# Kernel tuning notes

Hardware: AMD Instinct MI355X
Metric: run time of the kernel (lower is better)

The kernel has to match this reference:

```python
import jax, jax.numpy as jnp
import numpy as np

EPS = 1e-5
H = W = 14  # spatial grid, N = H*W = 196


def layernorm(x, g, b):
    m = x.mean(-1, keepdims=True)
    v = ((x - m) ** 2).mean(-1, keepdims=True)
    return (x - m) * jax.lax.rsqrt(v + EPS) * g + b


def fem_step(x, s):
    # x: [B, C, H, W]; blockwise instance-norm -> sigmoid gate -> 0.5*x + 0.5*attn*x
    B, C, h, w = x.shape
    nbh = -(-h // s)
    nbw = -(-w // s)
    idh = np.arange(h) // s
    idw = np.arange(w) // s
    bid_np = (idh[:, None] * nbw + idw[None, :]).reshape(-1)  # [h*w]
    cnt = jnp.asarray(np.bincount(bid_np, minlength=nbh * nbw).astype(np.float32))
    bid = jnp.asarray(bid_np)
    xt = x.reshape(B, C, h * w).transpose(2, 0, 1)  # [HW, B, C]
    s1 = jax.ops.segment_sum(xt, bid, num_segments=nbh * nbw)      # [nblk, B, C]
    s2 = jax.ops.segment_sum(xt * xt, bid, num_segments=nbh * nbw)
    mean = s1 / cnt[:, None, None]
    var = s2 / cnt[:, None, None] - mean * mean  # biased var, as F.instance_norm
    attn = jax.nn.sigmoid((xt - mean[bid]) * jax.lax.rsqrt(var[bid] + EPS))
    out = 0.5 * xt * (1.0 + attn)  # 0.5*x + 0.5*attn*x
    return out.transpose(1, 2, 0).reshape(B, C, h, w)


def fem(x):
    # p=[2,1,0] -> block sizes H//4=3, H//2=7, H//1=14
    for s in (H // 4, H // 2, H):
        x = fem_step(x, s)
    return x


def setup_inputs() -> dict:
    key = jax.random.key(0)
    ks = jax.random.split(key, 4)
    B, N, C = 64, H * W, 1024
    hid = 4 * C
    return {
        "x": jax.random.normal(ks[0], (B, N, C), jnp.float32),
        "ln1_g": jnp.ones((C,), jnp.float32),
        "ln1_b": jnp.zeros((C,), jnp.float32),
        "cw": jax.random.normal(ks[1], (H, W // 2 + 1, C, 2), jnp.float32) * 0.02,
        "ln2_g": jnp.ones((C,), jnp.float32),
        "ln2_b": jnp.zeros((C,), jnp.float32),
        "fc1_w": jax.random.normal(ks[2], (C, hid), jnp.float32) * 0.02,
        "fc1_b": jnp.zeros((hid,), jnp.float32),
        "fc2_w": jax.random.normal(ks[3], (hid, C), jnp.float32) * 0.02,
        "fc2_b": jnp.zeros((C,), jnp.float32),
    }


def reference(x, ln1_g, ln1_b, cw, ln2_g, ln2_b, fc1_w, fc1_b, fc2_w, fc2_b):
    B, N, C = x.shape
    # FFT global filter
    y = layernorm(x, ln1_g, ln1_b)
    yf = jnp.fft.rfft2(y.reshape(B, H, W, C), axes=(1, 2), norm="ortho")
    yf = yf * (cw[..., 0] + 1j * cw[..., 1])
    y = jnp.fft.irfft2(yf, s=(H, W), axes=(1, 2), norm="ortho").reshape(B, N, C)
    # MLP
    y = layernorm(y, ln2_g, ln2_b)
    y = jax.nn.gelu(y @ fc1_w + fc1_b, approximate=False) @ fc2_w + fc2_b
    # FEM on [B, C, H, W]
    y = fem(y.transpose(0, 2, 1).reshape(B, C, H, W))
    y = y.reshape(B, C, N).transpose(0, 2, 1)
    return x + y
```

## Files before the change

### kernel.cpp

```cpp
#include <hip/hip_runtime.h>

constexpr int CB = 64;
constexpr int CHH = 14, CWW = 14;
constexpr int CN = 196;
constexpr int CC = 1024;
constexpr int CROWS = CB * CN;
constexpr int CKW = 8;

constexpr float C14[14] = {
  1.0f, 0.9009688679024191f, 0.6234898018587336f, 0.2225209339563144f,
  -0.2225209339563144f, -0.6234898018587336f, -0.9009688679024191f, -1.0f,
  -0.9009688679024191f, -0.6234898018587336f, -0.2225209339563144f,
  0.2225209339563144f, 0.6234898018587336f, 0.9009688679024191f };
constexpr float S14[14] = {
  0.0f, 0.4338837391175581f, 0.7818314824680298f, 0.9749279121818236f,
  0.9749279121818236f, 0.7818314824680298f, 0.4338837391175581f, 0.0f,
  -0.4338837391175581f, -0.7818314824680298f, -0.9749279121818236f,
  -0.9749279121818236f, -0.7818314824680298f, -0.4338837391175581f };

typedef __attribute__((ext_vector_type(8))) short bf16x8;
typedef __attribute__((ext_vector_type(4))) float f32x4;

__device__ __forceinline__ unsigned short f2bf(float f) {
  unsigned u = __builtin_bit_cast(unsigned, f);
  u += 0x7FFFu + ((u >> 16) & 1u);
  return (unsigned short)(u >> 16);
}
__device__ __forceinline__ float bf2f(unsigned short h) {
  return __builtin_bit_cast(float, (unsigned)h << 16);
}

__device__ __forceinline__ void gload_lds16(const void* g, void* l) {
  __builtin_amdgcn_global_load_lds(
      (const __attribute__((address_space(1))) void*)g,
      (__attribute__((address_space(3))) void*)l, 16, 0, 0);
}

#define WAITV(N)  asm volatile("s_waitcnt vmcnt(" #N ")" ::: "memory")

template<int OUTBF>
__global__ __launch_bounds__(256)
void ln_kernel(const float* __restrict__ in, const float* __restrict__ gam,
               const float* __restrict__ bet, float* __restrict__ outf,
               unsigned short* __restrict__ outb)
{
  const int row = blockIdx.x;
  const int t = threadIdx.x;
  const float4 v = *(const float4*)(in + (size_t)row * CC + t * 4);
  float s  = v.x + v.y + v.z + v.w;
  float s2 = v.x*v.x + v.y*v.y + v.z*v.z + v.w*v.w;
  #pragma unroll
  for (int o = 32; o > 0; o >>= 1) { s += __shfl_down(s, o); s2 += __shfl_down(s2, o); }
  __shared__ float red[8];
  const int wid = t >> 6, lane = t & 63;
  if (lane == 0) { red[wid] = s; red[4 + wid] = s2; }
  __syncthreads();
  s  = red[0] + red[1] + red[2] + red[3];
  s2 = red[4] + red[5] + red[6] + red[7];
  const float mean = s * (1.0f / CC);
  const float var  = s2 * (1.0f / CC) - mean * mean;
  const float r = rsqrtf(var + 1e-5f);
  const float4 g4 = *(const float4*)(gam + t * 4);
  const float4 b4 = *(const float4*)(bet + t * 4);
  const float o0 = (v.x - mean) * r * g4.x + b4.x;
  const float o1 = (v.y - mean) * r * g4.y + b4.y;
  const float o2 = (v.z - mean) * r * g4.z + b4.z;
  const float o3 = (v.w - mean) * r * g4.w + b4.w;
  if (OUTBF) {
    ushort4 p; p.x = f2bf(o0); p.y = f2bf(o1); p.z = f2bf(o2); p.w = f2bf(o3);
    *(ushort4*)(outb + (size_t)row * CC + t * 4) = p;
  } else {
    *(float4*)(outf + (size_t)row * CC + t * 4) = make_float4(o0, o1, o2, o3);
  }
}

__global__ __launch_bounds__(256)
void fft_w_fwd(const float* __restrict__ y, float* __restrict__ Ar, float* __restrict__ Ai)
{
  const int t = threadIdx.x;
  const int bid = blockIdx.x;
  const int cc = bid & 3;
  const int tmp = bid >> 2;
  const int h = tmp % 14;
  const int b = tmp / 14;
  const int c = cc * 256 + t;
  const size_t base = ((size_t)b * CN + (size_t)h * CWW) * CC + c;
  float v[14];
  #pragma unroll
  for (int w = 0; w < 14; w++) v[w] = y[base + (size_t)w * CC];
  const size_t obase = (((size_t)b * CHH + h) * CKW) * CC + c;
  #pragma unroll
  for (int kw = 0; kw < 8; kw++) {
    float sr = 0.f, si = 0.f;
    #pragma unroll
    for (int w = 0; w < 14; w++) {
      const int m = (w * kw) % 14;
      sr += v[w] * C14[m];
      si -= v[w] * S14[m];
    }
    Ar[obase + (size_t)kw * CC] = sr;
    Ai[obase + (size_t)kw * CC] = si;
  }
}

__global__ __launch_bounds__(256)
void fft_h_filt(const float* __restrict__ Ar, const float* __restrict__ Ai,
                const float* __restrict__ cw, float* __restrict__ Br, float* __restrict__ Bi)
{
  const int t = threadIdx.x;
  const int bid = blockIdx.x;
  const int cc = bid & 3;
  const int tmp = bid >> 2;
  const int kw = tmp & 7;
  const int b = tmp >> 3;
  const int c = cc * 256 + t;
  const size_t base = (((size_t)b * CHH) * CKW + kw) * CC + c;
  float ar[14], ai[14];
  #pragma unroll
  for (int h = 0; h < 14; h++) {
    ar[h] = Ar[base + (size_t)h * (CKW * CC)];
    ai[h] = Ai[base + (size_t)h * (CKW * CC)];
  }
  float fr[14], fi[14];
  #pragma unroll
  for (int kh = 0; kh < 14; kh++) {
    float yr = 0.f, yi = 0.f;
    #pragma unroll
    for (int h = 0; h < 14; h++) {
      const int m = (h * kh) % 14;
      yr += ar[h] * C14[m] + ai[h] * S14[m];
      yi += ai[h] * C14[m] - ar[h] * S14[m];
    }
    const size_t widx = (((size_t)kh * CKW + kw) * CC + c) * 2;
    const float wr = cw[widx], wi = cw[widx + 1];
    fr[kh] = yr * wr - yi * wi;
    fi[kh] = yr * wi + yi * wr;
  }
  #pragma unroll
  for (int h = 0; h < 14; h++) {
    float sr = 0.f, si = 0.f;
    #pragma unroll
    for (int kh = 0; kh < 14; kh++) {
      const int m = (h * kh) % 14;
      sr += fr[kh] * C14[m] - fi[kh] * S14[m];
      si += fr[kh] * S14[m] + fi[kh] * C14[m];
    }
    Br[base + (size_t)h * (CKW * CC)] = sr;
    Bi[base + (size_t)h * (CKW * CC)] = si;
  }
}

__global__ __launch_bounds__(256)
void fft_w_inv(const float* __restrict__ Br, const float* __restrict__ Bi, float* __restrict__ y2)
{
  const int t = threadIdx.x;
  const int bid = blockIdx.x;
  const int cc = bid & 3;
  const int tmp = bid >> 2;
  const int h = tmp % 14;
  const int b = tmp / 14;
  const int c = cc * 256 + t;
  const size_t ibase = (((size_t)b * CHH + h) * CKW) * CC + c;
  float br[8], bi[8];
  #pragma unroll
  for (int k = 0; k < 8; k++) {
    br[k] = Br[ibase + (size_t)k * CC];
    bi[k] = Bi[ibase + (size_t)k * CC];
  }
  const size_t obase = ((size_t)b * CN + (size_t)h * CWW) * CC + c;
  #pragma unroll
  for (int w = 0; w < 14; w++) {
    float s = br[0] + ((w & 1) ? -br[7] : br[7]);
    #pragma unroll
    for (int k = 1; k < 7; k++) {
      const int m = (w * k) % 14;
      s += 2.0f * (br[k] * C14[m] - bi[k] * S14[m]);
    }
    y2[obase + (size_t)w * CC] = s * (1.0f / 196.0f);
  }
}

__global__ __launch_bounds__(256)
void transpose_f32_bf16(const float* __restrict__ in, unsigned short* __restrict__ out,
                        int R, int Ccols)
{
  __shared__ float tile[32][33];
  const int tx = threadIdx.x & 31;
  const int ty = threadIdx.x >> 5;
  const int cb = blockIdx.x * 32;
  const int rb = blockIdx.y * 32;
  #pragma unroll
  for (int i = 0; i < 32; i += 8)
    tile[ty + i][tx] = in[(size_t)(rb + ty + i) * Ccols + cb + tx];
  __syncthreads();
  #pragma unroll
  for (int i = 0; i < 32; i += 8)
    out[(size_t)(cb + ty + i) * R + rb + tx] = f2bf(tile[tx][ty + i]);
}

template<int DO_GELU>
__global__ __launch_bounds__(256, 4)
void gemm128(const unsigned short* __restrict__ A, const unsigned short* __restrict__ BT,
             const float* __restrict__ bias, unsigned short* __restrict__ C,
             int M, int N, int K)
{
  __shared__ __align__(16) char sA[8192];
  __shared__ __align__(16) char sB[8192];
  const int t = threadIdx.x;
  const int wid = t >> 6, lane = t & 63;
  const int wm = wid >> 1, wn = wid & 1;
  const int lrow = lane & 15, qk = lane >> 4;
  const int dq = qk << 4;

  const int nbx = N >> 7, nby = M >> 7;
  const int per = nbx << 3;
  const int fullg = nby >> 3;
  int by, bx;
  if ((int)blockIdx.x < fullg * per) {
    const int g = blockIdx.x / per, r = blockIdx.x % per;
    by = (g << 3) + (r & 7); bx = r >> 3;
  } else {
    const int r = blockIdx.x - fullg * per;
    const int rem = nby - (fullg << 3);
    by = (fullg << 3) + r % rem; bx = r / rem;
  }
  const int brow = by << 7, bcol = bx << 7;

  const int lr1  = t >> 3;
  const int pp   = (t & 7) << 4;
  const int s1   = pp ^ ((lr1 & 7) << 4);
  const int row1 = (lr1 << 1) + (s1 >> 6);
  const int col1 = (s1 & 63) >> 1;
  const size_t aoff1 = (size_t)(brow + row1) * K + col1;
  const size_t aoff2 = (size_t)(brow + row1 + 64) * K + col1;
  const size_t boff1 = (size_t)(bcol + row1) * K + col1;
  const size_t boff2 = (size_t)(bcol + row1 + 64) * K + col1;
  char* dstA1 = sA + t * 16; char* dstA2 = sA + 4096 + t * 16;
  char* dstB1 = sB + t * 16; char* dstB2 = sB + 4096 + t * 16;

  f32x4 acc[4][4] = {};

  for (int k0 = 0; k0 < K; k0 += 32) {
    __syncthreads();
    gload_lds16(A  + aoff1 + k0, dstA1);
    gload_lds16(A  + aoff2 + k0, dstA2);
    gload_lds16(BT + boff1 + k0, dstB1);
    gload_lds16(BT + boff2 + k0, dstB2);
    WAITV(0);
    __syncthreads();
    bf16x8 af[4], bf[4];
    #pragma unroll
    for (int mf = 0; mf < 4; ++mf) {
      const int row = wm * 64 + mf * 16 + lrow;
      af[mf] = *(const bf16x8*)(sA + (row >> 1) * 128 +
                ((((row & 1) << 6) | dq) ^ (((row >> 1) & 7) << 4)));
    }
    #pragma unroll
    for (int nf = 0; nf < 4; ++nf) {
      const int row = wn * 64 + nf * 16 + lrow;
      bf[nf] = *(const bf16x8*)(sB + (row >> 1) * 128 +
                ((((row & 1) << 6) | dq) ^ (((row >> 1) & 7) << 4)));
    }
    #pragma unroll
    for (int mf = 0; mf < 4; ++mf)
      #pragma unroll
      for (int nf = 0; nf < 4; ++nf)
        acc[mf][nf] = __builtin_amdgcn_mfma_f32_16x16x32_bf16(af[mf], bf[nf],
                                                              acc[mf][nf], 0, 0, 0);
  }

  #pragma unroll
  for (int mf = 0; mf < 4; ++mf) {
    #pragma unroll
    for (int nf = 0; nf < 4; ++nf) {
      const int ccol = bcol + wn * 64 + nf * 16 + lrow;
      const float bb = bias[ccol];
      #pragma unroll
      for (int j = 0; j < 4; ++j) {
        const int r = brow + wm * 64 + mf * 16 + qk * 4 + j;
        float v = acc[mf][nf][j] + bb;
        if (DO_GELU) v = 0.5f * v * (1.0f + erff(v * 0.70710678118654752f));
        C[(size_t)r * N + ccol] = f2bf(v);
      }
    }
  }
}

__device__ __forceinline__ void fem_block(unsigned short* col, int t,
                                          int h0, int nh, int w0, int nw)
{
  float s = 0.f, s2 = 0.f;
  for (int ih = 0; ih < nh; ih++)
    for (int iw = 0; iw < nw; iw++) {
      const float v = bf2f(col[((h0 + ih) * 14 + w0 + iw) * 128 + t]);
      s += v; s2 += v * v;
    }
  const float inv = 1.0f / (float)(nh * nw);
  const float m = s * inv;
  const float var = s2 * inv - m * m;
  const float r = rsqrtf(var + 1e-5f);
  for (int ih = 0; ih < nh; ih++)
    for (int iw = 0; iw < nw; iw++) {
      const int idx = ((h0 + ih) * 14 + w0 + iw) * 128 + t;
      const float v = bf2f(col[idx]);
      const float a = 1.0f / (1.0f + __expf(-(v - m) * r));
      col[idx] = f2bf(0.5f * v * (1.0f + a));
    }
}

__global__ __launch_bounds__(128)
void fem_kernel(const unsigned short* __restrict__ z, const float* __restrict__ x,
                float* __restrict__ out)
{
  __shared__ unsigned short buf[CN * 128];
  const int t = threadIdx.x;
  const int b = blockIdx.x >> 3;
  const int cc = blockIdx.x & 7;
  const int c = cc * 128 + t;
  const size_t base = (size_t)b * CN * CC + c;
  #pragma unroll 4
  for (int n = 0; n < CN; n++) buf[n * 128 + t] = z[base + (size_t)n * CC];
  const int st3[5] = {0, 3, 6, 9, 12};
  const int ln3[5] = {3, 3, 3, 3, 2};
  for (int i = 0; i < 5; i++)
    for (int j = 0; j < 5; j++)
      fem_block(buf, t, st3[i], ln3[i], st3[j], ln3[j]);
  for (int i = 0; i < 2; i++)
    for (int j = 0; j < 2; j++)
      fem_block(buf, t, i * 7, 7, j * 7, 7);
  fem_block(buf, t, 0, 14, 0, 14);
  #pragma unroll 4
  for (int n = 0; n < CN; n++)
    out[base + (size_t)n * CC] = x[base + (size_t)n * CC] + bf2f(buf[n * 128 + t]);
}

extern "C" void kernel_launch(void* const* d_in, const int* in_sizes, int n_in,
                              void* d_out, int out_size, void* d_ws, size_t ws_size,
                              hipStream_t stream) {
  const float* x     = (const float*)d_in[0];
  const float* ln1_g = (const float*)d_in[1];
  const float* ln1_b = (const float*)d_in[2];
  const float* cw    = (const float*)d_in[3];
  const float* ln2_g = (const float*)d_in[4];
  const float* ln2_b = (const float*)d_in[5];
  const float* fc1_w = (const float*)d_in[6];
  const float* fc1_b = (const float*)d_in[7];
  const float* fc2_w = (const float*)d_in[8];
  const float* fc2_b = (const float*)d_in[9];
  float* out = (float*)d_out;
  char* ws = (char*)d_ws;

  const size_t SZ_A = (size_t)CB * CHH * CKW * CC * 4;
  float* Ar = (float*)(ws);
  float* Ai = (float*)(ws + SZ_A);
  float* Br = (float*)(ws + 2 * SZ_A);
  float* Bi = (float*)(ws + 3 * SZ_A);
  unsigned short* A1   = (unsigned short*)(ws);
  unsigned short* W1T  = (unsigned short*)(ws + SZ_A);
  unsigned short* W2T  = (unsigned short*)(ws + SZ_A + (size_t)4096 * 1024 * 2);
  unsigned short* Hmid = (unsigned short*)(ws + 2 * SZ_A);
  unsigned short* Z    = (unsigned short*)(ws);

  ln_kernel<0><<<CROWS, 256, 0, stream>>>(x, ln1_g, ln1_b, out, nullptr);
  fft_w_fwd<<<CB * CHH * 4, 256, 0, stream>>>(out, Ar, Ai);
  fft_h_filt<<<CB * CKW * 4, 256, 0, stream>>>(Ar, Ai, cw, Br, Bi);
  fft_w_inv<<<CB * CHH * 4, 256, 0, stream>>>(Br, Bi, out);
  ln_kernel<1><<<CROWS, 256, 0, stream>>>(out, ln2_g, ln2_b, nullptr, A1);
  transpose_f32_bf16<<<dim3(4096 / 32, 1024 / 32), 256, 0, stream>>>(fc1_w, W1T, 1024, 4096);
  transpose_f32_bf16<<<dim3(1024 / 32, 4096 / 32), 256, 0, stream>>>(fc2_w, W2T, 4096, 1024);
  gemm128<1><<<dim3(3136), 256, 0, stream>>>(A1, W1T, fc1_b, Hmid, CROWS, 4096, 1024);
  gemm128<0><<<dim3(784), 256, 0, stream>>>(Hmid, W2T, fc2_b, Z, CROWS, 1024, 4096);
  fem_kernel<<<CB * 8, 128, 0, stream>>>(Z, x, out);
}
```

Measured before the change: 504.7 us.

## Store FFT intermediates in bf16 and use 128x64 tiles for fc2 GEMM

The layernorm, FFT stages and inverse FFT now read and write bf16 intermediates instead of fp32, which halves the memory traffic of the spectral filter pipeline. The workspace layout is rearranged to match. A new 128x64-tile GEMM kernel doubles the block count for the fc2 projection (784 to 1568 blocks) so more CUs stay busy. The cost is extra rounding error in the FFT path.

```diff
diff --git a/kernel.cpp b/kernel.cpp
--- a/kernel.cpp
+++ b/kernel.cpp
@@ -38,15 +38,20 @@
 
 #define WAITV(N)  asm volatile("s_waitcnt vmcnt(" #N ")" ::: "memory")
 
-template<int OUTBF>
+template<int INBF>
 __global__ __launch_bounds__(256)
-void ln_kernel(const float* __restrict__ in, const float* __restrict__ gam,
-               const float* __restrict__ bet, float* __restrict__ outf,
-               unsigned short* __restrict__ outb)
+void ln_kernel(const void* __restrict__ in_, const float* __restrict__ gam,
+               const float* __restrict__ bet, unsigned short* __restrict__ outb)
 {
   const int row = blockIdx.x;
   const int t = threadIdx.x;
-  const float4 v = *(const float4*)(in + (size_t)row * CC + t * 4);
+  float4 v;
+  if (INBF) {
+    const ushort4 u = ((const ushort4*)in_)[(size_t)row * 256 + t];
+    v = make_float4(bf2f(u.x), bf2f(u.y), bf2f(u.z), bf2f(u.w));
+  } else {
+    v = ((const float4*)in_)[(size_t)row * 256 + t];
+  }
   float s  = v.x + v.y + v.z + v.w;
   float s2 = v.x*v.x + v.y*v.y + v.z*v.z + v.w*v.w;
   #pragma unroll
@@ -62,20 +67,17 @@
   const float r = rsqrtf(var + 1e-5f);
   const float4 g4 = *(const float4*)(gam + t * 4);
   const float4 b4 = *(const float4*)(bet + t * 4);
-  const float o0 = (v.x - mean) * r * g4.x + b4.x;
-  const float o1 = (v.y - mean) * r * g4.y + b4.y;
-  const float o2 = (v.z - mean) * r * g4.z + b4.z;
-  const float o3 = (v.w - mean) * r * g4.w + b4.w;
-  if (OUTBF) {
-    ushort4 p; p.x = f2bf(o0); p.y = f2bf(o1); p.z = f2bf(o2); p.w = f2bf(o3);
-    *(ushort4*)(outb + (size_t)row * CC + t * 4) = p;
-  } else {
-    *(float4*)(outf + (size_t)row * CC + t * 4) = make_float4(o0, o1, o2, o3);
-  }
+  ushort4 p;
+  p.x = f2bf((v.x - mean) * r * g4.x + b4.x);
+  p.y = f2bf((v.y - mean) * r * g4.y + b4.y);
+  p.z = f2bf((v.z - mean) * r * g4.z + b4.z);
+  p.w = f2bf((v.w - mean) * r * g4.w + b4.w);
+  *(ushort4*)(outb + (size_t)row * CC + t * 4) = p;
 }
 
 __global__ __launch_bounds__(256)
-void fft_w_fwd(const float* __restrict__ y, float* __restrict__ Ar, float* __restrict__ Ai)
+void fft_w_fwd(const unsigned short* __restrict__ y,
+               unsigned short* __restrict__ Ar, unsigned short* __restrict__ Ai)
 {
   const int t = threadIdx.x;
   const int bid = blockIdx.x;
@@ -87,7 +89,7 @@
   const size_t base = ((size_t)b * CN + (size_t)h * CWW) * CC + c;
   float v[14];
   #pragma unroll
-  for (int w = 0; w < 14; w++) v[w] = y[base + (size_t)w * CC];
+  for (int w = 0; w < 14; w++) v[w] = bf2f(y[base + (size_t)w * CC]);
   const size_t obase = (((size_t)b * CHH + h) * CKW) * CC + c;
   #pragma unroll
   for (int kw = 0; kw < 8; kw++) {
@@ -98,14 +100,15 @@
       sr += v[w] * C14[m];
       si -= v[w] * S14[m];
     }
-    Ar[obase + (size_t)kw * CC] = sr;
-    Ai[obase + (size_t)kw * CC] = si;
+    Ar[obase + (size_t)kw * CC] = f2bf(sr);
+    Ai[obase + (size_t)kw * CC] = f2bf(si);
   }
 }
 
 __global__ __launch_bounds__(256)
-void fft_h_filt(const float* __restrict__ Ar, const float* __restrict__ Ai,
-                const float* __restrict__ cw, float* __restrict__ Br, float* __restrict__ Bi)
+void fft_h_filt(const unsigned short* __restrict__ Ar, const unsigned short* __restrict__ Ai,
+                const float* __restrict__ cw,
+                unsigned short* __restrict__ Br, unsigned short* __restrict__ Bi)
 {
   const int t = threadIdx.x;
   const int bid = blockIdx.x;
@@ -118,8 +121,8 @@
   float ar[14], ai[14];
   #pragma unroll
   for (int h = 0; h < 14; h++) {
-    ar[h] = Ar[base + (size_t)h * (CKW * CC)];
-    ai[h] = Ai[base + (size_t)h * (CKW * CC)];
+    ar[h] = bf2f(Ar[base + (size_t)h * (CKW * CC)]);
+    ai[h] = bf2f(Ai[base + (size_t)h * (CKW * CC)]);
   }
   float fr[14], fi[14];
   #pragma unroll
@@ -145,13 +148,14 @@
       sr += fr[kh] * C14[m] - fi[kh] * S14[m];
       si += fr[kh] * S14[m] + fi[kh] * C14[m];
     }
-    Br[base + (size_t)h * (CKW * CC)] = sr;
-    Bi[base + (size_t)h * (CKW * CC)] = si;
+    Br[base + (size_t)h * (CKW * CC)] = f2bf(sr);
+    Bi[base + (size_t)h * (CKW * CC)] = f2bf(si);
   }
 }
 
 __global__ __launch_bounds__(256)
-void fft_w_inv(const float* __restrict__ Br, const float* __restrict__ Bi, float* __restrict__ y2)
+void fft_w_inv(const unsigned short* __restrict__ Br, const unsigned short* __restrict__ Bi,
+               unsigned short* __restrict__ y2)
 {
   const int t = threadIdx.x;
   const int bid = blockIdx.x;
@@ -164,8 +168,8 @@
   float br[8], bi[8];
   #pragma unroll
   for (int k = 0; k < 8; k++) {
-    br[k] = Br[ibase + (size_t)k * CC];
-    bi[k] = Bi[ibase + (size_t)k * CC];
+    br[k] = bf2f(Br[ibase + (size_t)k * CC]);
+    bi[k] = bf2f(Bi[ibase + (size_t)k * CC]);
   }
   const size_t obase = ((size_t)b * CN + (size_t)h * CWW) * CC + c;
   #pragma unroll
@@ -176,7 +180,7 @@
       const int m = (w * k) % 14;
       s += 2.0f * (br[k] * C14[m] - bi[k] * S14[m]);
     }
-    y2[obase + (size_t)w * CC] = s * (1.0f / 196.0f);
+    y2[obase + (size_t)w * CC] = f2bf(s * (1.0f / 196.0f));
   }
 }
 
@@ -281,6 +285,89 @@
         float v = acc[mf][nf][j] + bb;
         if (DO_GELU) v = 0.5f * v * (1.0f + erff(v * 0.70710678118654752f));
         C[(size_t)r * N + ccol] = f2bf(v);
+      }
+    }
+  }
+}
+
+__global__ __launch_bounds__(256, 6)
+void gemm128x64(const unsigned short* __restrict__ A, const unsigned short* __restrict__ BT,
+                const float* __restrict__ bias, unsigned short* __restrict__ C,
+                int M, int N, int K)
+{
+  __shared__ __align__(16) char sA[8192];
+  __shared__ __align__(16) char sB[4096];
+  const int t = threadIdx.x;
+  const int wid = t >> 6, lane = t & 63;
+  const int wm = wid >> 1, wn = wid & 1;
+  const int lrow = lane & 15, qk = lane >> 4;
+  const int dq = qk << 4;
+
+  const int nbx = N >> 6, nby = M >> 7;
+  const int per = nbx << 2;
+  const int fullg = nby >> 2;
+  int by, bx;
+  if ((int)blockIdx.x < fullg * per) {
+    const int g = blockIdx.x / per, r = blockIdx.x % per;
+    by = (g << 2) + (r & 3); bx = r >> 2;
+  } else {
+    const int r = blockIdx.x - fullg * per;
+    const int rem = nby - (fullg << 2);
+    by = (fullg << 2) + r % rem; bx = r / rem;
+  }
+  const int brow = by << 7, bcol = bx << 6;
+
+  const int lr1  = t >> 3;
+  const int pp   = (t & 7) << 4;
+  const int s1   = pp ^ ((lr1 & 7) << 4);
+  const int row1 = (lr1 << 1) + (s1 >> 6);
+  const int col1 = (s1 & 63) >> 1;
+  const size_t aoff1 = (size_t)(brow + row1) * K + col1;
+  const size_t aoff2 = (size_t)(brow + row1 + 64) * K + col1;
+  const size_t boff1 = (size_t)(bcol + row1) * K + col1;
+  char* dstA1 = sA + t * 16; char* dstA2 = sA + 4096 + t * 16;
+  char* dstB1 = sB + t * 16;
+
+  f32x4 acc[4][2] = {};
+
+  for (int k0 = 0; k0 < K; k0 += 32) {
+    __syncthreads();
+    gload_lds16(A  + aoff1 + k0, dstA1);
+    gload_lds16(A  + aoff2 + k0, dstA2);
+    gload_lds16(BT + boff1 + k0, dstB1);
+    WAITV(0);
+    __syncthreads();
+    bf16x8 af[4], bf[2];
+    #pragma unroll
+    for (int mf = 0; mf < 4; ++mf) {
+      const int row = wm * 64 + mf * 16 + lrow;
+      af[mf] = *(const bf16x8*)(sA + (row >> 1) * 128 +
+                ((((row & 1) << 6) | dq) ^ (((row >> 1) & 7) << 4)));
+    }
+    #pragma unroll
+    for (int nf = 0; nf < 2; ++nf) {
+      const int row = wn * 32 + nf * 16 + lrow;
+      bf[nf] = *(const bf16x8*)(sB + (row >> 1) * 128 +
+                ((((row & 1) << 6) | dq) ^ (((row >> 1) & 7) << 4)));
+    }
+    #pragma unroll
+    for (int mf = 0; mf < 4; ++mf)
+      #pragma unroll
+      for (int nf = 0; nf < 2; ++nf)
+        acc[mf][nf] = __builtin_amdgcn_mfma_f32_16x16x32_bf16(af[mf], bf[nf],
+                                                              acc[mf][nf], 0, 0, 0);
+  }
+
+  #pragma unroll
+  for (int mf = 0; mf < 4; ++mf) {
+    #pragma unroll
+    for (int nf = 0; nf < 2; ++nf) {
+      const int ccol = bcol + wn * 32 + nf * 16 + lrow;
+      const float bb = bias[ccol];
+      #pragma unroll
+      for (int j = 0; j < 4; ++j) {
+        const int r = brow + wm * 64 + mf * 16 + qk * 4 + j;
+        C[(size_t)r * N + ccol] = f2bf(acc[mf][nf][j] + bb);
       }
     }
   }
@@ -350,25 +437,26 @@
   float* out = (float*)d_out;
   char* ws = (char*)d_ws;
 
-  const size_t SZ_A = (size_t)CB * CHH * CKW * CC * 4;
-  float* Ar = (float*)(ws);
-  float* Ai = (float*)(ws + SZ_A);
-  float* Br = (float*)(ws + 2 * SZ_A);
-  float* Bi = (float*)(ws + 3 * SZ_A);
+  const size_t S = (size_t)CB * CHH * CKW * CC * 2;
+  unsigned short* Ar = (unsigned short*)(ws);
+  unsigned short* Ai = (unsigned short*)(ws + S);
+  unsigned short* Br = (unsigned short*)(ws + 2 * S);
+  unsigned short* Bi = (unsigned short*)(ws + 3 * S);
   unsigned short* A1   = (unsigned short*)(ws);
-  unsigned short* W1T  = (unsigned short*)(ws + SZ_A);
-  unsigned short* W2T  = (unsigned short*)(ws + SZ_A + (size_t)4096 * 1024 * 2);
-  unsigned short* Hmid = (unsigned short*)(ws + 2 * SZ_A);
+  unsigned short* W1T  = (unsigned short*)(ws + 2 * S);
+  unsigned short* W2T  = (unsigned short*)(ws + 2 * S + (size_t)4096 * 1024 * 2);
+  unsigned short* Hmid = (unsigned short*)(ws + 2 * S + (size_t)4096 * 1024 * 4);
   unsigned short* Z    = (unsigned short*)(ws);
-
-  ln_kernel<0><<<CROWS, 256, 0, stream>>>(x, ln1_g, ln1_b, out, nullptr);
-  fft_w_fwd<<<CB * CHH * 4, 256, 0, stream>>>(out, Ar, Ai);
+  unsigned short* y12  = (unsigned short*)d_out;
+
+  ln_kernel<0><<<CROWS, 256, 0, stream>>>(x, ln1_g, ln1_b, y12);
+  fft_w_fwd<<<CB * CHH * 4, 256, 0, stream>>>(y12, Ar, Ai);
   fft_h_filt<<<CB * CKW * 4, 256, 0, stream>>>(Ar, Ai, cw, Br, Bi);
-  fft_w_inv<<<CB * CHH * 4, 256, 0, stream>>>(Br, Bi, out);
-  ln_kernel<1><<<CROWS, 256, 0, stream>>>(out, ln2_g, ln2_b, nullptr, A1);
+  fft_w_inv<<<CB * CHH * 4, 256, 0, stream>>>(Br, Bi, y12);
+  ln_kernel<1><<<CROWS, 256, 0, stream>>>(y12, ln2_g, ln2_b, A1);
   transpose_f32_bf16<<<dim3(4096 / 32, 1024 / 32), 256, 0, stream>>>(fc1_w, W1T, 1024, 4096);
   transpose_f32_bf16<<<dim3(1024 / 32, 4096 / 32), 256, 0, stream>>>(fc2_w, W2T, 4096, 1024);
   gemm128<1><<<dim3(3136), 256, 0, stream>>>(A1, W1T, fc1_b, Hmid, CROWS, 4096, 1024);
-  gemm128<0><<<dim3(784), 256, 0, stream>>>(Hmid, W2T, fc2_b, Z, CROWS, 1024, 4096);
+  gemm128x64<<<dim3(1568), 256, 0, stream>>>(Hmid, W2T, fc2_b, Z, CROWS, 1024, 4096);
   fem_kernel<<<CB * 8, 128, 0, stream>>>(Z, x, out);
 }
```

Result: slower. 524.5 us (+3.9%).

## Store FFT intermediates in packed bf16 and deepen GEMM K-tile to 64

Applied to the files above, without the earlier changes.

The layernorm and FFT stages now keep their intermediates in bf16, with real and imaginary parts packed into one 32-bit word. Each thread handles 4 or 2 channels with vector loads, and fewer blocks are launched. The aim is to roughly halve the memory traffic of the memory-bound FFT and layernorm pipeline. Separately, the GEMM stages 64-wide K tiles in double-size LDS with a new swizzle, which halves the loop iterations and barriers. In exchange, FFT precision drops to bf16, and the larger LDS footprint may reduce GEMM occupancy.

```diff
diff --git a/kernel.cpp b/kernel.cpp
--- a/kernel.cpp
+++ b/kernel.cpp
@@ -29,6 +29,9 @@
 __device__ __forceinline__ float bf2f(unsigned short h) {
   return __builtin_bit_cast(float, (unsigned)h << 16);
 }
+__device__ __forceinline__ unsigned pack2(float re, float im) {
+  return (unsigned)f2bf(re) | ((unsigned)f2bf(im) << 16);
+}
 
 __device__ __forceinline__ void gload_lds16(const void* g, void* l) {
   __builtin_amdgcn_global_load_lds(
@@ -38,15 +41,20 @@
 
 #define WAITV(N)  asm volatile("s_waitcnt vmcnt(" #N ")" ::: "memory")
 
-template<int OUTBF>
-__global__ __launch_bounds__(256)
-void ln_kernel(const float* __restrict__ in, const float* __restrict__ gam,
-               const float* __restrict__ bet, float* __restrict__ outf,
-               unsigned short* __restrict__ outb)
+template<int INBF>
+__global__ __launch_bounds__(256)
+void ln_kernel(const void* __restrict__ in_, const float* __restrict__ gam,
+               const float* __restrict__ bet, unsigned short* __restrict__ outb)
 {
   const int row = blockIdx.x;
   const int t = threadIdx.x;
-  const float4 v = *(const float4*)(in + (size_t)row * CC + t * 4);
+  float4 v;
+  if (INBF) {
+    const ushort4 u = ((const ushort4*)in_)[(size_t)row * 256 + t];
+    v = make_float4(bf2f(u.x), bf2f(u.y), bf2f(u.z), bf2f(u.w));
+  } else {
+    v = ((const float4*)in_)[(size_t)row * 256 + t];
+  }
   float s  = v.x + v.y + v.z + v.w;
   float s2 = v.x*v.x + v.y*v.y + v.z*v.z + v.w*v.w;
   #pragma unroll
@@ -62,121 +70,139 @@
   const float r = rsqrtf(var + 1e-5f);
   const float4 g4 = *(const float4*)(gam + t * 4);
   const float4 b4 = *(const float4*)(bet + t * 4);
-  const float o0 = (v.x - mean) * r * g4.x + b4.x;
-  const float o1 = (v.y - mean) * r * g4.y + b4.y;
-  const float o2 = (v.z - mean) * r * g4.z + b4.z;
-  const float o3 = (v.w - mean) * r * g4.w + b4.w;
-  if (OUTBF) {
-    ushort4 p; p.x = f2bf(o0); p.y = f2bf(o1); p.z = f2bf(o2); p.w = f2bf(o3);
-    *(ushort4*)(outb + (size_t)row * CC + t * 4) = p;
-  } else {
-    *(float4*)(outf + (size_t)row * CC + t * 4) = make_float4(o0, o1, o2, o3);
-  }
-}
-
-__global__ __launch_bounds__(256)
-void fft_w_fwd(const float* __restrict__ y, float* __restrict__ Ar, float* __restrict__ Ai)
+  ushort4 p;
+  p.x = f2bf((v.x - mean) * r * g4.x + b4.x);
+  p.y = f2bf((v.y - mean) * r * g4.y + b4.y);
+  p.z = f2bf((v.z - mean) * r * g4.z + b4.z);
+  p.w = f2bf((v.w - mean) * r * g4.w + b4.w);
+  *(ushort4*)(outb + (size_t)row * CC + t * 4) = p;
+}
+
+__global__ __launch_bounds__(256)
+void fft_w_fwd(const unsigned short* __restrict__ y, unsigned* __restrict__ Az)
 {
   const int t = threadIdx.x;
   const int bid = blockIdx.x;
-  const int cc = bid & 3;
-  const int tmp = bid >> 2;
-  const int h = tmp % 14;
-  const int b = tmp / 14;
-  const int c = cc * 256 + t;
-  const size_t base = ((size_t)b * CN + (size_t)h * CWW) * CC + c;
-  float v[14];
-  #pragma unroll
-  for (int w = 0; w < 14; w++) v[w] = y[base + (size_t)w * CC];
-  const size_t obase = (((size_t)b * CHH + h) * CKW) * CC + c;
+  const int h = bid % 14;
+  const int b = bid / 14;
+  const int c4 = t * 4;
+  const size_t base = ((size_t)b * CN + (size_t)h * CWW) * CC + c4;
+  float v[14][4];
+  #pragma unroll
+  for (int w = 0; w < 14; w++) {
+    const ushort4 u = *(const ushort4*)(y + base + (size_t)w * CC);
+    v[w][0] = bf2f(u.x); v[w][1] = bf2f(u.y); v[w][2] = bf2f(u.z); v[w][3] = bf2f(u.w);
+  }
+  const size_t obase = (((size_t)b * CHH + h) * CKW) * CC + c4;
   #pragma unroll
   for (int kw = 0; kw < 8; kw++) {
-    float sr = 0.f, si = 0.f;
+    float sr[4] = {}, si[4] = {};
     #pragma unroll
     for (int w = 0; w < 14; w++) {
       const int m = (w * kw) % 14;
-      sr += v[w] * C14[m];
-      si -= v[w] * S14[m];
-    }
-    Ar[obase + (size_t)kw * CC] = sr;
-    Ai[obase + (size_t)kw * CC] = si;
-  }
-}
-
-__global__ __launch_bounds__(256)
-void fft_h_filt(const float* __restrict__ Ar, const float* __restrict__ Ai,
-                const float* __restrict__ cw, float* __restrict__ Br, float* __restrict__ Bi)
+      #pragma unroll
+      for (int j = 0; j < 4; j++) {
+        sr[j] += v[w][j] * C14[m];
+        si[j] -= v[w][j] * S14[m];
+      }
+    }
+    uint4 o;
+    o.x = pack2(sr[0], si[0]); o.y = pack2(sr[1], si[1]);
+    o.z = pack2(sr[2], si[2]); o.w = pack2(sr[3], si[3]);
+    *(uint4*)(Az + obase + (size_t)kw * CC) = o;
+  }
+}
+
+__global__ __launch_bounds__(256)
+void fft_h_filt(const unsigned* __restrict__ Az, const float* __restrict__ cw,
+                unsigned* __restrict__ Bz)
 {
   const int t = threadIdx.x;
   const int bid = blockIdx.x;
-  const int cc = bid & 3;
-  const int tmp = bid >> 2;
+  const int half = bid & 1;
+  const int tmp = bid >> 1;
   const int kw = tmp & 7;
   const int b = tmp >> 3;
-  const int c = cc * 256 + t;
-  const size_t base = (((size_t)b * CHH) * CKW + kw) * CC + c;
-  float ar[14], ai[14];
+  const int c2 = half * 512 + t * 2;
+  const size_t base = (((size_t)b * CHH) * CKW + kw) * CC + c2;
+  float ar[14][2], ai[14][2];
   #pragma unroll
   for (int h = 0; h < 14; h++) {
-    ar[h] = Ar[base + (size_t)h * (CKW * CC)];
-    ai[h] = Ai[base + (size_t)h * (CKW * CC)];
-  }
-  float fr[14], fi[14];
+    const uint2 u = *(const uint2*)(Az + base + (size_t)h * (CKW * CC));
+    ar[h][0] = bf2f((unsigned short)(u.x & 0xffff)); ai[h][0] = bf2f((unsigned short)(u.x >> 16));
+    ar[h][1] = bf2f((unsigned short)(u.y & 0xffff)); ai[h][1] = bf2f((unsigned short)(u.y >> 16));
+  }
+  float fr[14][2], fi[14][2];
   #pragma unroll
   for (int kh = 0; kh < 14; kh++) {
-    float yr = 0.f, yi = 0.f;
+    float yr[2] = {}, yi[2] = {};
     #pragma unroll
     for (int h = 0; h < 14; h++) {
       const int m = (h * kh) % 14;
-      yr += ar[h] * C14[m] + ai[h] * S14[m];
-      yi += ai[h] * C14[m] - ar[h] * S14[m];
-    }
-    const size_t widx = (((size_t)kh * CKW + kw) * CC + c) * 2;
-    const float wr = cw[widx], wi = cw[widx + 1];
-    fr[kh] = yr * wr - yi * wi;
-    fi[kh] = yr * wi + yi * wr;
+      #pragma unroll
+      for (int j = 0; j < 2; j++) {
+        yr[j] += ar[h][j] * C14[m] + ai[h][j] * S14[m];
+        yi[j] += ai[h][j] * C14[m] - ar[h][j] * S14[m];
+      }
+    }
+    const float4 w4 = *(const float4*)(cw + ((size_t)(kh * CKW + kw) * CC + c2) * 2);
+    fr[kh][0] = yr[0] * w4.x - yi[0] * w4.y; fi[kh][0] = yr[0] * w4.y + yi[0] * w4.x;
+    fr[kh][1] = yr[1] * w4.z - yi[1] * w4.w; fi[kh][1] = yr[1] * w4.w + yi[1] * w4.z;
   }
   #pragma unroll
   for (int h = 0; h < 14; h++) {
-    float sr = 0.f, si = 0.f;
+    float sr[2] = {}, si[2] = {};
     #pragma unroll
     for (int kh = 0; kh < 14; kh++) {
       const int m = (h * kh) % 14;
-      sr += fr[kh] * C14[m] - fi[kh] * S14[m];
-      si += fr[kh] * S14[m] + fi[kh] * C14[m];
-    }
-    Br[base + (size_t)h * (CKW * CC)] = sr;
-    Bi[base + (size_t)h * (CKW * CC)] = si;
-  }
-}
-
-__global__ __launch_bounds__(256)
-void fft_w_inv(const float* __restrict__ Br, const float* __restrict__ Bi, float* __restrict__ y2)
+      #pragma unroll
+      for (int j = 0; j < 2; j++) {
+        sr[j] += fr[kh][j] * C14[m] - fi[kh][j] * S14[m];
+        si[j] += fr[kh][j] * S14[m] + fi[kh][j] * C14[m];
+      }
+    }
+    uint2 o;
+    o.x = pack2(sr[0], si[0]); o.y = pack2(sr[1], si[1]);
+    *(uint2*)(Bz + base + (size_t)h * (CKW * CC)) = o;
+  }
+}
+
+__global__ __launch_bounds__(256)
+void fft_w_inv(const unsigned* __restrict__ Bz, unsigned short* __restrict__ y2)
 {
   const int t = threadIdx.x;
   const int bid = blockIdx.x;
-  const int cc = bid & 3;
-  const int tmp = bid >> 2;
-  const int h = tmp % 14;
-  const int b = tmp / 14;
-  const int c = cc * 256 + t;
-  const size_t ibase = (((size_t)b * CHH + h) * CKW) * CC + c;
-  float br[8], bi[8];
+  const int h = bid % 14;
+  const int b = bid / 14;
+  const int c4 = t * 4;
+  const size_t ibase = (((size_t)b * CHH + h) * CKW) * CC + c4;
+  float br[8][4], bi[8][4];
   #pragma unroll
   for (int k = 0; k < 8; k++) {
-    br[k] = Br[ibase + (size_t)k * CC];
-    bi[k] = Bi[ibase + (size_t)k * CC];
-  }
-  const size_t obase = ((size_t)b * CN + (size_t)h * CWW) * CC + c;
+    const uint4 u = *(const uint4*)(Bz + ibase + (size_t)k * CC);
+    br[k][0] = bf2f((unsigned short)(u.x & 0xffff)); bi[k][0] = bf2f((unsigned short)(u.x >> 16));
+    br[k][1] = bf2f((unsigned short)(u.y & 0xffff)); bi[k][1] = bf2f((unsigned short)(u.y >> 16));
+    br[k][2] = bf2f((unsigned short)(u.z & 0xffff)); bi[k][2] = bf2f((unsigned short)(u.z >> 16));
+    br[k][3] = bf2f((unsigned short)(u.w & 0xffff)); bi[k][3] = bf2f((unsigned short)(u.w >> 16));
+  }
+  const size_t obase = ((size_t)b * CN + (size_t)h * CWW) * CC + c4;
   #pragma unroll
   for (int w = 0; w < 14; w++) {
-    float s = br[0] + ((w & 1) ? -br[7] : br[7]);
+    float s[4];
+    #pragma unroll
+    for (int j = 0; j < 4; j++)
+      s[j] = br[0][j] + ((w & 1) ? -br[7][j] : br[7][j]);
     #pragma unroll
     for (int k = 1; k < 7; k++) {
       const int m = (w * k) % 14;
-      s += 2.0f * (br[k] * C14[m] - bi[k] * S14[m]);
-    }
-    y2[obase + (size_t)w * CC] = s * (1.0f / 196.0f);
+      #pragma unroll
+      for (int j = 0; j < 4; j++)
+        s[j] += 2.0f * (br[k][j] * C14[m] - bi[k][j] * S14[m]);
+    }
+    ushort4 o;
+    o.x = f2bf(s[0] * (1.0f / 196.0f)); o.y = f2bf(s[1] * (1.0f / 196.0f));
+    o.z = f2bf(s[2] * (1.0f / 196.0f)); o.w = f2bf(s[3] * (1.0f / 196.0f));
+    *(ushort4*)(y2 + obase + (size_t)w * CC) = o;
   }
 }
 
@@ -204,8 +230,8 @@
              const float* __restrict__ bias, unsigned short* __restrict__ C,
              int M, int N, int K)
 {
-  __shared__ __align__(16) char sA[8192];
-  __shared__ __align__(16) char sB[8192];
+  __shared__ __align__(16) char sA[16384];
+  __shared__ __align__(16) char sB[16384];
   const int t = threadIdx.x;
   const int wid = t >> 6, lane = t & 63;
   const int wm = wid >> 1, wn = wid & 1;
@@ -226,47 +252,41 @@
   }
   const int brow = by << 7, bcol = bx << 7;
 
-  const int lr1  = t >> 3;
-  const int pp   = (t & 7) << 4;
-  const int s1   = pp ^ ((lr1 & 7) << 4);
-  const int row1 = (lr1 << 1) + (s1 >> 6);
-  const int col1 = (s1 & 63) >> 1;
-  const size_t aoff1 = (size_t)(brow + row1) * K + col1;
-  const size_t aoff2 = (size_t)(brow + row1 + 64) * K + col1;
-  const size_t boff1 = (size_t)(bcol + row1) * K + col1;
-  const size_t boff2 = (size_t)(bcol + row1 + 64) * K + col1;
-  char* dstA1 = sA + t * 16; char* dstA2 = sA + 4096 + t * 16;
-  char* dstB1 = sB + t * 16; char* dstB2 = sB + 4096 + t * 16;
+  const int vr = t >> 3;
+  const int cl = ((t ^ (t >> 3)) & 7) << 3;
+  const int dstb = t * 16;
 
   f32x4 acc[4][4] = {};
 
-  for (int k0 = 0; k0 < K; k0 += 32) {
+  for (int k0 = 0; k0 < K; k0 += 64) {
     __syncthreads();
-    gload_lds16(A  + aoff1 + k0, dstA1);
-    gload_lds16(A  + aoff2 + k0, dstA2);
-    gload_lds16(BT + boff1 + k0, dstB1);
-    gload_lds16(BT + boff2 + k0, dstB2);
+    #pragma unroll
+    for (int i = 0; i < 4; ++i) {
+      gload_lds16(A  + (size_t)(brow + i * 32 + vr) * K + k0 + cl, sA + i * 4096 + dstb);
+      gload_lds16(BT + (size_t)(bcol + i * 32 + vr) * K + k0 + cl, sB + i * 4096 + dstb);
+    }
     WAITV(0);
     __syncthreads();
-    bf16x8 af[4], bf[4];
-    #pragma unroll
-    for (int mf = 0; mf < 4; ++mf) {
-      const int row = wm * 64 + mf * 16 + lrow;
-      af[mf] = *(const bf16x8*)(sA + (row >> 1) * 128 +
-                ((((row & 1) << 6) | dq) ^ (((row >> 1) & 7) << 4)));
-    }
-    #pragma unroll
-    for (int nf = 0; nf < 4; ++nf) {
-      const int row = wn * 64 + nf * 16 + lrow;
-      bf[nf] = *(const bf16x8*)(sB + (row >> 1) * 128 +
-                ((((row & 1) << 6) | dq) ^ (((row >> 1) & 7) << 4)));
-    }
-    #pragma unroll
-    for (int mf = 0; mf < 4; ++mf)
-      #pragma unroll
-      for (int nf = 0; nf < 4; ++nf)
-        acc[mf][nf] = __builtin_amdgcn_mfma_f32_16x16x32_bf16(af[mf], bf[nf],
-                                                              acc[mf][nf], 0, 0, 0);
+    #pragma unroll
+    for (int ks = 0; ks < 2; ++ks) {
+      bf16x8 af[4], bf[4];
+      #pragma unroll
+      for (int mf = 0; mf < 4; ++mf) {
+        const int row = wm * 64 + mf * 16 + lrow;
+        af[mf] = *(const bf16x8*)(sA + row * 128 + (((ks << 6) | dq) ^ ((row & 7) << 4)));
+      }
+      #pragma unroll
+      for (int nf = 0; nf < 4; ++nf) {
+        const int row = wn * 64 + nf * 16 + lrow;
+        bf[nf] = *(const bf16x8*)(sB + row * 128 + (((ks << 6) | dq) ^ ((row & 7) << 4)));
+      }
+      #pragma unroll
+      for (int mf = 0; mf < 4; ++mf)
+        #pragma unroll
+        for (int nf = 0; nf < 4; ++nf)
+          acc[mf][nf] = __builtin_amdgcn_mfma_f32_16x16x32_bf16(af[mf], bf[nf],
+                                                                acc[mf][nf], 0, 0, 0);
+    }
   }
 
   #pragma unroll
@@ -350,22 +370,21 @@
   float* out = (float*)d_out;
   char* ws = (char*)d_ws;
 
-  const size_t SZ_A = (size_t)CB * CHH * CKW * CC * 4;
-  float* Ar = (float*)(ws);
-  float* Ai = (float*)(ws + SZ_A);
-  float* Br = (float*)(ws + 2 * SZ_A);
-  float* Bi = (float*)(ws + 3 * SZ_A);
+  const size_t SZ = (size_t)CB * CHH * CKW * CC * 4;
+  unsigned* Az = (unsigned*)(ws);
+  unsigned* Bz = (unsigned*)(ws + SZ);
   unsigned short* A1   = (unsigned short*)(ws);
-  unsigned short* W1T  = (unsigned short*)(ws + SZ_A);
-  unsigned short* W2T  = (unsigned short*)(ws + SZ_A + (size_t)4096 * 1024 * 2);
-  unsigned short* Hmid = (unsigned short*)(ws + 2 * SZ_A);
+  unsigned short* W1T  = (unsigned short*)(ws + SZ);
+  unsigned short* W2T  = (unsigned short*)(ws + SZ + (size_t)4096 * 1024 * 2);
+  unsigned short* Hmid = (unsigned short*)(ws + SZ + (size_t)4096 * 1024 * 4);
   unsigned short* Z    = (unsigned short*)(ws);
-
-  ln_kernel<0><<<CROWS, 256, 0, stream>>>(x, ln1_g, ln1_b, out, nullptr);
-  fft_w_fwd<<<CB * CHH * 4, 256, 0, stream>>>(out, Ar, Ai);
-  fft_h_filt<<<CB * CKW * 4, 256, 0, stream>>>(Ar, Ai, cw, Br, Bi);
-  fft_w_inv<<<CB * CHH * 4, 256, 0, stream>>>(Br, Bi, out);
-  ln_kernel<1><<<CROWS, 256, 0, stream>>>(out, ln2_g, ln2_b, nullptr, A1);
+  unsigned short* y12  = (unsigned short*)d_out;
+
+  ln_kernel<0><<<CROWS, 256, 0, stream>>>(x, ln1_g, ln1_b, y12);
+  fft_w_fwd<<<CB * CHH, 256, 0, stream>>>(y12, Az);
+  fft_h_filt<<<CB * CKW * 2, 256, 0, stream>>>(Az, cw, Bz);
+  fft_w_inv<<<CB * CHH, 256, 0, stream>>>(Bz, y12);
+  ln_kernel<1><<<CROWS, 256, 0, stream>>>(y12, ln2_g, ln2_b, A1);
   transpose_f32_bf16<<<dim3(4096 / 32, 1024 / 32), 256, 0, stream>>>(fc1_w, W1T, 1024, 4096);
   transpose_f32_bf16<<<dim3(1024 / 32, 4096 / 32), 256, 0, stream>>>(fc2_w, W2T, 4096, 1024);
   gemm128<1><<<dim3(3136), 256, 0, stream>>>(A1, W1T, fc1_b, Hmid, CROWS, 4096, 1024);
```

After: 459.3 us. -9.0%, faster.
